# Kernel tuning notes

Measured on AMD Instinct MI355X. Metric: run time of the kernel, lower is better.

The kernel has to match this reference:

```python
import jax, jax.numpy as jnp
import numpy as np

N_ATOMS = 1_000_000
N_GRAPHS = 8192
FEA_DIM = 64
HIDDEN = 32
N_HEAD = 3


def setup_inputs() -> dict:
    key = jax.random.key(0)
    k1, k2, k3, k4, k5, k6 = jax.random.split(key, 6)
    atom_feas = jax.random.normal(k1, (N_ATOMS, FEA_DIM), dtype=jnp.float32)
    atom_owner = jnp.sort(jax.random.randint(k2, (N_ATOMS,), 0, N_GRAPHS))
    s1 = 1.0 / np.sqrt(FEA_DIM)
    s2 = 1.0 / np.sqrt(HIDDEN)
    W1 = jax.random.uniform(k3, (FEA_DIM, HIDDEN), jnp.float32, -s1, s1)
    b1 = jax.random.uniform(k4, (HIDDEN,), jnp.float32, -s1, s1)
    W2 = jax.random.uniform(k5, (HIDDEN, N_HEAD), jnp.float32, -s2, s2)
    b2 = jax.random.uniform(k6, (N_HEAD,), jnp.float32, -s2, s2)
    return {"atom_feas": atom_feas, "atom_owner": atom_owner,
            "W1": W1, "b1": b1, "W2": W2, "b2": b2}


def reference(atom_feas, atom_owner, W1, b1, W2, b2):
    # key MLP: Linear -> SiLU -> Linear, producing per-atom, per-head logits [N, H]
    h = jax.nn.silu(atom_feas @ W1 + b1)
    logits = h @ W2 + b2  # [N, H]
    # per-graph (segment) softmax over atoms, independently per head
    seg_max = jax.ops.segment_max(logits, atom_owner, num_segments=N_GRAPHS)  # [G, H]
    e = jnp.exp(logits - seg_max[atom_owner])
    denom = jax.ops.segment_sum(e, atom_owner, num_segments=N_GRAPHS)  # [G, H]
    w = e / denom[atom_owner]  # [N, H]
    # attention-weighted pooling: per graph, atom_fea.T @ w -> [D, H] flattened row-major
    outer = (atom_feas[:, :, None] * w[:, None, :]).reshape(atom_feas.shape[0], FEA_DIM * N_HEAD)
    crystal_feas = jax.ops.segment_sum(outer, atom_owner, num_segments=N_GRAPHS)  # [G, D*H]
    return crystal_feas
```

## Files before the change

kernel.cpp:

```cpp
#include <hip/hip_runtime.h>
#include <math.h>
#include <stdint.h>

#define NFEA   64
#define NHEAD  3
#define GPB    4
#define LCAP   256

typedef float v2f __attribute__((ext_vector_type(2)));

__device__ __forceinline__ void wave_sync_lds() {
  asm volatile("s_waitcnt lgkmcnt(0)" ::: "memory");
}

__global__ void gar_starts(const int* __restrict__ owner, int* __restrict__ starts,
                           int n_atoms, int n_graphs)
{
  int a = blockIdx.x * blockDim.x + threadIdx.x;
  if (a >= n_atoms) return;
  int cur  = owner[a];
  int prev = (a == 0) ? -1 : owner[a - 1];
  for (int g = prev + 1; g <= cur; ++g) starts[g] = a;
  if (a == n_atoms - 1)
    for (int g = cur + 1; g <= n_graphs; ++g) starts[g] = n_atoms;
}

__global__ __launch_bounds__(256, 4) void gar_mlp(
    const float* __restrict__ atom_feas,
    const float* __restrict__ W1, const float* __restrict__ b1,
    const float* __restrict__ W2, const float* __restrict__ b2,
    float4* __restrict__ logits4, int n_atoms)
{
  const int a = blockIdx.x * 256 + threadIdx.x;
  if (a >= n_atoms) return;
  const float4* __restrict__ xrow = (const float4*)(atom_feas + (size_t)a * NFEA);

  float4 xr[16];
#pragma unroll
  for (int q = 0; q < 16; ++q) xr[q] = xrow[q];

  v2f h[16];
#pragma unroll
  for (int j = 0; j < 16; ++j) h[j] = ((const v2f*)b1)[j];

#pragma unroll
  for (int q = 0; q < 16; ++q) {
    float xs[4] = {xr[q].x, xr[q].y, xr[q].z, xr[q].w};
#pragma unroll
    for (int dd = 0; dd < 4; ++dd) {
      v2f xd2 = {xs[dd], xs[dd]};
      const v2f* wrow = ((const v2f*)W1) + (q * 4 + dd) * 16;
#pragma unroll
      for (int jj = 0; jj < 16; ++jj)
        h[jj] = __builtin_elementwise_fma(xd2, wrow[jj], h[jj]);
    }
  }

  float l0 = b2[0], l1 = b2[1], l2 = b2[2];
#pragma unroll
  for (int jj = 0; jj < 16; ++jj) {
#pragma unroll
    for (int cc = 0; cc < 2; ++cc) {
      float hj = h[jj][cc];
      float s = hj * __builtin_amdgcn_rcpf(1.0f + __expf(-hj));
      int k = 2 * jj + cc;
      l0 = fmaf(s, W2[k * 3 + 0], l0);
      l1 = fmaf(s, W2[k * 3 + 1], l1);
      l2 = fmaf(s, W2[k * 3 + 2], l2);
    }
  }
  logits4[a] = make_float4(l0, l1, l2, 0.f);
}

__global__ __launch_bounds__(GPB * 64, 8) void gar_pool(
    const float* __restrict__ atom_feas,
    const int*   __restrict__ starts,
    const float4* __restrict__ logits4,
    float* __restrict__ out, int n_graphs)
{
  __shared__ __align__(16) float4 e4[GPB][LCAP];
  const int w = threadIdx.x >> 6, t = threadIdx.x & 63;
  const int g = blockIdx.x * GPB + w;
  if (g >= n_graphs) return;
  const int s0 = starts[g];
  const int n  = starts[g + 1] - s0;
  float* __restrict__ outg = out + (size_t)g * (NFEA * NHEAD);
  if (n <= 0) {
    outg[t * 3 + 0] = 0.f; outg[t * 3 + 1] = 0.f; outg[t * 3 + 2] = 0.f;
    return;
  }

  float lr[4][3];
  float m0 = -INFINITY, m1 = -INFINITY, m2 = -INFINITY;
#pragma unroll
  for (int c = 0; c < 4; ++c) {
    if (c * 64 < n) {
      int i = c * 64 + t;
      bool act = i < n;
      float4 lv = logits4[s0 + (act ? i : 0)];
      lr[c][0] = act ? lv.x : -INFINITY;
      lr[c][1] = act ? lv.y : -INFINITY;
      lr[c][2] = act ? lv.z : -INFINITY;
      m0 = fmaxf(m0, lr[c][0]); m1 = fmaxf(m1, lr[c][1]); m2 = fmaxf(m2, lr[c][2]);
    } else {
      lr[c][0] = -INFINITY; lr[c][1] = -INFINITY; lr[c][2] = -INFINITY;
    }
  }
  for (int i = 4 * 64 + t; i < n; i += 64) {
    float4 lv = logits4[s0 + i];
    m0 = fmaxf(m0, lv.x); m1 = fmaxf(m1, lv.y); m2 = fmaxf(m2, lv.z);
  }
#pragma unroll
  for (int off = 32; off > 0; off >>= 1) {
    m0 = fmaxf(m0, __shfl_xor(m0, off));
    m1 = fmaxf(m1, __shfl_xor(m1, off));
    m2 = fmaxf(m2, __shfl_xor(m2, off));
  }

  float d0 = 0.f, d1 = 0.f, d2 = 0.f;
#pragma unroll
  for (int c = 0; c < 4; ++c) {
    if (c * 64 < n) {
      float e0 = __expf(lr[c][0] - m0);
      float e1 = __expf(lr[c][1] - m1);
      float e2 = __expf(lr[c][2] - m2);
      d0 += e0; d1 += e1; d2 += e2;
      e4[w][c * 64 + t] = make_float4(e0, e1, e2, 0.f);
    }
  }
  for (int i = 4 * 64 + t; i < n; i += 64) {
    float4 lv = logits4[s0 + i];
    d0 += __expf(lv.x - m0); d1 += __expf(lv.y - m1); d2 += __expf(lv.z - m2);
  }
#pragma unroll
  for (int off = 32; off > 0; off >>= 1) {
    d0 += __shfl_xor(d0, off);
    d1 += __shfl_xor(d1, off);
    d2 += __shfl_xor(d2, off);
  }
  wave_sync_lds();

  float a0 = 0.f, a1 = 0.f, a2 = 0.f;
  const float* __restrict__ xcol = atom_feas + (size_t)s0 * NFEA + t;
  const int nmain = n < LCAP ? n : LCAP;
#pragma unroll 4
  for (int a = 0; a < nmain; ++a) {
    float  xv = xcol[(size_t)a * NFEA];
    float4 ev = e4[w][a];
    a0 = fmaf(ev.x, xv, a0);
    a1 = fmaf(ev.y, xv, a1);
    a2 = fmaf(ev.z, xv, a2);
  }
  for (int a = LCAP; a < n; ++a) {
    float4 lv = logits4[s0 + a];
    float  xv = xcol[(size_t)a * NFEA];
    a0 = fmaf(__expf(lv.x - m0), xv, a0);
    a1 = fmaf(__expf(lv.y - m1), xv, a1);
    a2 = fmaf(__expf(lv.z - m2), xv, a2);
  }

  const float i0 = 1.f / d0, i1 = 1.f / d1, i2 = 1.f / d2;
  outg[t * 3 + 0] = a0 * i0;
  outg[t * 3 + 1] = a1 * i1;
  outg[t * 3 + 2] = a2 * i2;
}

extern "C" void kernel_launch(void* const* d_in, const int* in_sizes, int n_in,
                              void* d_out, int out_size, void* d_ws, size_t ws_size,
                              hipStream_t stream)
{
  const float* atom_feas = (const float*)d_in[0];
  const int*   owner     = (const int*)d_in[1];
  const float* W1        = (const float*)d_in[2];
  const float* b1        = (const float*)d_in[3];
  const float* W2        = (const float*)d_in[4];
  const float* b2        = (const float*)d_in[5];
  float* out = (float*)d_out;

  const int n_atoms  = in_sizes[1];
  const int n_graphs = out_size / (NFEA * NHEAD);

  int* starts = (int*)d_ws;
  const size_t log_off = (((size_t)(n_graphs + 1) * sizeof(int)) + 255) & ~(size_t)255;
  float4* logits4 = (float4*)((char*)d_ws + log_off);

  hipLaunchKernelGGL(gar_starts, dim3((n_atoms + 255) / 256), dim3(256), 0, stream,
                     owner, starts, n_atoms, n_graphs);
  hipLaunchKernelGGL(gar_mlp, dim3((n_atoms + 255) / 256), dim3(256), 0, stream,
                     atom_feas, W1, b1, W2, b2, logits4, n_atoms);
  hipLaunchKernelGGL(gar_pool, dim3((n_graphs + GPB - 1) / GPB), dim3(GPB * 64), 0, stream,
                     atom_feas, starts, logits4, out, n_graphs);
}
```

Baseline: 418.3 us.

## Fuse MLP and segment pooling per atom block using atomics, drop max pass

Merges the per-atom MLP and the per-graph pooling into one kernel. Each 256-atom block computes exp(logit) without a max shift, stages the results in LDS, and atomically adds partial weighted sums and denominators for every graph it overlaps. A final kernel divides by the accumulated denominators. This removes the logits round-trip and the second full pass over atom_feas, since the pooling re-reads rows the block just loaded. In exchange it adds atomic traffic, zero-fill memsets and an extra launch. Dropping the max subtraction can overflow if logits are large.

```diff
diff --git a/kernel.cpp b/kernel.cpp
--- a/kernel.cpp
+++ b/kernel.cpp
@@ -4,14 +4,8 @@
 
 #define NFEA   64
 #define NHEAD  3
-#define GPB    4
-#define LCAP   256
 
 typedef float v2f __attribute__((ext_vector_type(2)));
-
-__device__ __forceinline__ void wave_sync_lds() {
-  asm volatile("s_waitcnt lgkmcnt(0)" ::: "memory");
-}
 
 __global__ void gar_starts(const int* __restrict__ owner, int* __restrict__ starts,
                            int n_atoms, int n_graphs)
@@ -25,16 +19,24 @@
     for (int g = cur + 1; g <= n_graphs; ++g) starts[g] = n_atoms;
 }
 
-__global__ __launch_bounds__(256, 4) void gar_mlp(
+__global__ __launch_bounds__(256, 4) void gar_fused(
     const float* __restrict__ atom_feas,
+    const int*   __restrict__ owner,
+    const int*   __restrict__ starts,
     const float* __restrict__ W1, const float* __restrict__ b1,
     const float* __restrict__ W2, const float* __restrict__ b2,
-    float4* __restrict__ logits4, int n_atoms)
+    float* __restrict__ out,
+    float* __restrict__ denom,
+    int n_atoms)
 {
-  const int a = blockIdx.x * 256 + threadIdx.x;
-  if (a >= n_atoms) return;
-  const float4* __restrict__ xrow = (const float4*)(atom_feas + (size_t)a * NFEA);
+  __shared__ __align__(16) float4 e4[256];
+  const int tid = threadIdx.x;
+  const int blockstart = blockIdx.x * 256;
+  const int a = blockstart + tid;
+  const bool act = a < n_atoms;
+  const int ar = act ? a : n_atoms - 1;
 
+  const float4* __restrict__ xrow = (const float4*)(atom_feas + (size_t)ar * NFEA);
   float4 xr[16];
 #pragma unroll
   for (int q = 0; q < 16; ++q) xr[q] = xrow[q];
@@ -55,7 +57,6 @@
         h[jj] = __builtin_elementwise_fma(xd2, wrow[jj], h[jj]);
     }
   }
-
   float l0 = b2[0], l1 = b2[1], l2 = b2[2];
 #pragma unroll
   for (int jj = 0; jj < 16; ++jj) {
@@ -69,100 +70,54 @@
       l2 = fmaf(s, W2[k * 3 + 2], l2);
     }
   }
-  logits4[a] = make_float4(l0, l1, l2, 0.f);
+  const float e0 = act ? __expf(l0) : 0.f;
+  const float e1 = act ? __expf(l1) : 0.f;
+  const float e2 = act ? __expf(l2) : 0.f;
+  e4[tid] = make_float4(e0, e1, e2, 0.f);
+  __syncthreads();
+
+  const int blockend = (blockstart + 256 < n_atoms) ? blockstart + 256 : n_atoms;
+  const int g0 = owner[blockstart];
+  const int g1 = owner[blockend - 1];
+  const int w = tid >> 6, t = tid & 63;
+
+  for (int g = g0; g <= g1; ++g) {
+    int lo = starts[g];     if (lo < blockstart) lo = blockstart;
+    int hi = starts[g + 1]; if (hi > blockend)   hi = blockend;
+    if (lo >= hi) continue;
+
+    float a0 = 0.f, a1 = 0.f, a2 = 0.f;
+    float dd0 = 0.f, dd1 = 0.f, dd2 = 0.f;
+    for (int i = lo + w; i < hi; i += 4) {
+      float4 ev = e4[i - blockstart];
+      float xv = atom_feas[(size_t)i * NFEA + t];
+      a0 = fmaf(ev.x, xv, a0);
+      a1 = fmaf(ev.y, xv, a1);
+      a2 = fmaf(ev.z, xv, a2);
+      dd0 += ev.x; dd1 += ev.y; dd2 += ev.z;
+    }
+    float* og = out + (size_t)g * (NFEA * NHEAD) + t * 3;
+    atomicAdd(og + 0, a0);
+    atomicAdd(og + 1, a1);
+    atomicAdd(og + 2, a2);
+    if (t == 0) {
+      atomicAdd(&denom[g * 3 + 0], dd0);
+      atomicAdd(&denom[g * 3 + 1], dd1);
+      atomicAdd(&denom[g * 3 + 2], dd2);
+    }
+  }
 }
 
-__global__ __launch_bounds__(GPB * 64, 8) void gar_pool(
-    const float* __restrict__ atom_feas,
-    const int*   __restrict__ starts,
-    const float4* __restrict__ logits4,
-    float* __restrict__ out, int n_graphs)
+__global__ void gar_norm(float* __restrict__ out, const float* __restrict__ denom,
+                         int total)
 {
-  __shared__ __align__(16) float4 e4[GPB][LCAP];
-  const int w = threadIdx.x >> 6, t = threadIdx.x & 63;
-  const int g = blockIdx.x * GPB + w;
-  if (g >= n_graphs) return;
-  const int s0 = starts[g];
-  const int n  = starts[g + 1] - s0;
-  float* __restrict__ outg = out + (size_t)g * (NFEA * NHEAD);
-  if (n <= 0) {
-    outg[t * 3 + 0] = 0.f; outg[t * 3 + 1] = 0.f; outg[t * 3 + 2] = 0.f;
-    return;
-  }
-
-  float lr[4][3];
-  float m0 = -INFINITY, m1 = -INFINITY, m2 = -INFINITY;
-#pragma unroll
-  for (int c = 0; c < 4; ++c) {
-    if (c * 64 < n) {
-      int i = c * 64 + t;
-      bool act = i < n;
-      float4 lv = logits4[s0 + (act ? i : 0)];
-      lr[c][0] = act ? lv.x : -INFINITY;
-      lr[c][1] = act ? lv.y : -INFINITY;
-      lr[c][2] = act ? lv.z : -INFINITY;
-      m0 = fmaxf(m0, lr[c][0]); m1 = fmaxf(m1, lr[c][1]); m2 = fmaxf(m2, lr[c][2]);
-    } else {
-      lr[c][0] = -INFINITY; lr[c][1] = -INFINITY; lr[c][2] = -INFINITY;
-    }
-  }
-  for (int i = 4 * 64 + t; i < n; i += 64) {
-    float4 lv = logits4[s0 + i];
-    m0 = fmaxf(m0, lv.x); m1 = fmaxf(m1, lv.y); m2 = fmaxf(m2, lv.z);
-  }
-#pragma unroll
-  for (int off = 32; off > 0; off >>= 1) {
-    m0 = fmaxf(m0, __shfl_xor(m0, off));
-    m1 = fmaxf(m1, __shfl_xor(m1, off));
-    m2 = fmaxf(m2, __shfl_xor(m2, off));
-  }
-
-  float d0 = 0.f, d1 = 0.f, d2 = 0.f;
-#pragma unroll
-  for (int c = 0; c < 4; ++c) {
-    if (c * 64 < n) {
-      float e0 = __expf(lr[c][0] - m0);
-      float e1 = __expf(lr[c][1] - m1);
-      float e2 = __expf(lr[c][2] - m2);
-      d0 += e0; d1 += e1; d2 += e2;
-      e4[w][c * 64 + t] = make_float4(e0, e1, e2, 0.f);
-    }
-  }
-  for (int i = 4 * 64 + t; i < n; i += 64) {
-    float4 lv = logits4[s0 + i];
-    d0 += __expf(lv.x - m0); d1 += __expf(lv.y - m1); d2 += __expf(lv.z - m2);
-  }
-#pragma unroll
-  for (int off = 32; off > 0; off >>= 1) {
-    d0 += __shfl_xor(d0, off);
-    d1 += __shfl_xor(d1, off);
-    d2 += __shfl_xor(d2, off);
-  }
-  wave_sync_lds();
-
-  float a0 = 0.f, a1 = 0.f, a2 = 0.f;
-  const float* __restrict__ xcol = atom_feas + (size_t)s0 * NFEA + t;
-  const int nmain = n < LCAP ? n : LCAP;
-#pragma unroll 4
-  for (int a = 0; a < nmain; ++a) {
-    float  xv = xcol[(size_t)a * NFEA];
-    float4 ev = e4[w][a];
-    a0 = fmaf(ev.x, xv, a0);
-    a1 = fmaf(ev.y, xv, a1);
-    a2 = fmaf(ev.z, xv, a2);
-  }
-  for (int a = LCAP; a < n; ++a) {
-    float4 lv = logits4[s0 + a];
-    float  xv = xcol[(size_t)a * NFEA];
-    a0 = fmaf(__expf(lv.x - m0), xv, a0);
-    a1 = fmaf(__expf(lv.y - m1), xv, a1);
-    a2 = fmaf(__expf(lv.z - m2), xv, a2);
-  }
-
-  const float i0 = 1.f / d0, i1 = 1.f / d1, i2 = 1.f / d2;
-  outg[t * 3 + 0] = a0 * i0;
-  outg[t * 3 + 1] = a1 * i1;
-  outg[t * 3 + 2] = a2 * i2;
+  int i = blockIdx.x * 256 + threadIdx.x;
+  if (i >= total) return;
+  int g = i / (NFEA * NHEAD);
+  int h = i % NHEAD;
+  float dn = denom[g * 3 + h];
+  float v = out[i];
+  out[i] = dn > 0.f ? v / dn : 0.f;
 }
 
 extern "C" void kernel_launch(void* const* d_in, const int* in_sizes, int n_in,
@@ -181,13 +136,16 @@
   const int n_graphs = out_size / (NFEA * NHEAD);
 
   int* starts = (int*)d_ws;
-  const size_t log_off = (((size_t)(n_graphs + 1) * sizeof(int)) + 255) & ~(size_t)255;
-  float4* logits4 = (float4*)((char*)d_ws + log_off);
+  const size_t den_off = (((size_t)(n_graphs + 1) * sizeof(int)) + 255) & ~(size_t)255;
+  float* denom = (float*)((char*)d_ws + den_off);
+
+  hipMemsetAsync(out, 0, (size_t)out_size * sizeof(float), stream);
+  hipMemsetAsync(denom, 0, (size_t)n_graphs * 3 * sizeof(float), stream);
 
   hipLaunchKernelGGL(gar_starts, dim3((n_atoms + 255) / 256), dim3(256), 0, stream,
                      owner, starts, n_atoms, n_graphs);
-  hipLaunchKernelGGL(gar_mlp, dim3((n_atoms + 255) / 256), dim3(256), 0, stream,
-                     atom_feas, W1, b1, W2, b2, logits4, n_atoms);
-  hipLaunchKernelGGL(gar_pool, dim3((n_graphs + GPB - 1) / GPB), dim3(GPB * 64), 0, stream,
-                     atom_feas, starts, logits4, out, n_graphs);
+  hipLaunchKernelGGL(gar_fused, dim3((n_atoms + 255) / 256), dim3(256), 0, stream,
+                     atom_feas, owner, starts, W1, b1, W2, b2, out, denom, n_atoms);
+  hipLaunchKernelGGL(gar_norm, dim3((out_size + 255) / 256), dim3(256), 0, stream,
+                     out, denom, out_size);
 }
```

Result: slower. 482.4 us (+15.3%).
